# Kernel tuning notes

Measured on AMD Instinct MI355X. Metric: run time of the kernel, lower is better.

## Reference

```python
import jax, jax.numpy as jnp
import numpy as np

N, E, G = 50000, 1600000, 8
IN, H, C = 64, 4, 32
HID = H * C  # 128
L = 3


def setup_inputs() -> dict:
    key = jax.random.key(0)
    ks = jax.random.split(key, 20)
    x = jax.random.normal(ks[0], (N, IN), dtype=jnp.float32)
    edge_index = jax.random.randint(ks[1], (2, E), 0, N, dtype=jnp.int64)
    batch = jnp.sort(jax.random.randint(ks[2], (N,), 0, G, dtype=jnp.int64))
    s = 0.05
    Wp = jax.random.normal(ks[3], (IN, HID), dtype=jnp.float32) * s
    bp = jnp.zeros((HID,), dtype=jnp.float32)
    Wl = jax.random.normal(ks[4], (L, HID, HID), dtype=jnp.float32) * s
    att_src = jax.random.normal(ks[5], (L, H, C), dtype=jnp.float32) * s
    att_dst = jax.random.normal(ks[6], (L, H, C), dtype=jnp.float32) * s
    bconv = jnp.zeros((L, HID), dtype=jnp.float32)
    W1 = jax.random.normal(ks[7], (2 * HID, 256), dtype=jnp.float32) * s
    b1 = jnp.zeros((256,), dtype=jnp.float32)
    W2 = jax.random.normal(ks[8], (256, 128), dtype=jnp.float32) * s
    b2 = jnp.zeros((128,), dtype=jnp.float32)
    W3 = jax.random.normal(ks[9], (128, 1), dtype=jnp.float32) * s
    b3 = jnp.zeros((1,), dtype=jnp.float32)
    return dict(x=x, edge_index=edge_index, batch=batch, Wp=Wp, bp=bp, Wl=Wl,
                att_src=att_src, att_dst=att_dst, bconv=bconv,
                W1=W1, b1=b1, W2=W2, b2=b2, W3=W3, b3=b3)


def _gat_layer(x, src, dst, W, a_src, a_dst, b):
    # PyG GATConv (concat=True, add_self_loops handled by caller via src/dst)
    h = (x @ W).reshape(N, H, C)                      # [N,H,C]
    asrc = jnp.sum(h * a_src, axis=-1)                # [N,H]
    adst = jnp.sum(h * a_dst, axis=-1)                # [N,H]
    e = jax.nn.leaky_relu(asrc[src] + adst[dst], 0.2)  # [E',H]
    m = jax.ops.segment_max(e, dst, num_segments=N)   # scatter-softmax over dst
    e = jnp.exp(e - m[dst])
    z = jax.ops.segment_sum(e, dst, num_segments=N)
    alpha = e / (z[dst] + 1e-16)                      # [E',H]
    out = jax.ops.segment_sum(h[src] * alpha[:, :, None], dst, num_segments=N)
    return out.reshape(N, HID) + b


def reference(x, edge_index, batch, Wp, bp, Wl, att_src, att_dst, bconv,
              W1, b1, W2, b2, W3, b3):
    # add self loops once (PyG default add_self_loops=True)
    loop = jnp.arange(N, dtype=edge_index.dtype)
    src = jnp.concatenate([edge_index[0], loop])
    dst = jnp.concatenate([edge_index[1], loop])

    h = jax.nn.relu(x @ Wp + bp)
    for l in range(L):
        h = jax.nn.relu(_gat_layer(h, src, dst, Wl[l], att_src[l], att_dst[l], bconv[l]))

    cnt = jax.ops.segment_sum(jnp.ones((N,), h.dtype), batch, num_segments=G)
    mean = jax.ops.segment_sum(h, batch, num_segments=G) / jnp.maximum(cnt, 1.0)[:, None]
    mx = jax.ops.segment_max(h, batch, num_segments=G)
    mx = jnp.where(cnt[:, None] > 0, mx, 0.0)
    p = jnp.concatenate([mean, mx], axis=-1)          # [G, 2*HID]

    p = jax.nn.relu(p @ W1 + b1)
    p = jax.nn.relu(p @ W2 + b2)
    return (p @ W3 + b3).squeeze(-1)                  # [G]
```

## Files before the change

### kernel.cpp

```cpp
#include <hip/hip_runtime.h>
#include <math.h>

#define NN 50000
#define GG 8
#define HEADS 4
#define CH 32
#define HID 128
#define NLAYER 3
#define POOL_S 64
#define DEG_CAP 96
#define NBG2 ((NN + 63) / 64)
#define NBS 1024

__device__ float g_h[(size_t)NN * HID];
__device__ float g_h2[(size_t)NN * HID];
__device__ unsigned short g_h2b[(size_t)NN * HID];
__device__ float g_as[(size_t)NN * HEADS];
__device__ float g_ad[(size_t)NN * HEADS];
__device__ int g_cursor[NN];
__device__ unsigned short g_csr16[(size_t)NN * DEG_CAP];
__device__ int g_starts[GG + 1];
__device__ double g_psum[(size_t)GG * POOL_S * HID];
__device__ float g_pmax[(size_t)GG * POOL_S * HID];

__device__ __forceinline__ float lrelu(float v) { return v > 0.f ? v : 0.2f * v; }

__device__ __forceinline__ float bf2f(unsigned short u) {
    union { unsigned int i; float f; } v;
    v.i = ((unsigned int)u) << 16;
    return v.f;
}
__device__ __forceinline__ unsigned short f2bf(float f) {
    union { float f; unsigned int i; } v;
    v.f = f;
    unsigned int r = v.i + 0x7FFFu + ((v.i >> 16) & 1u);
    return (unsigned short)(r >> 16);
}

__global__ void zero_kernel() {
    int i = blockIdx.x * blockDim.x + threadIdx.x;
    if (i < NN) g_cursor[i] = 0;
}

template <int K, bool ATT, bool RELU, bool SRC_PARAM>
__device__ __forceinline__ void gemm_body(
    const float* __restrict__ Xp, const float* __restrict__ W, const float* __restrict__ bias,
    const float* __restrict__ att_s, const float* __restrict__ att_d, int n, int blk) {
    constexpr int KT = 32;
    constexpr int XS = 68;
    __shared__ float Ws[KT * 128];
    __shared__ float Xs[KT * XS];
    const float* X = SRC_PARAM ? Xp : g_h;
    float* Y = ATT ? g_h2 : g_h;
    int tid = threadIdx.x;
    int base = blk * 64;
    int rows = n - base;
    if (rows > 64) rows = 64;
    int cg = tid & 15, rg = tid >> 4;
    int c0 = cg * 8, r0 = rg * 4;
    float acc[4][8];
#pragma unroll
    for (int i = 0; i < 4; i++)
#pragma unroll
        for (int j = 0; j < 8; j++) acc[i][j] = 0.f;

    for (int kb = 0; kb < K; kb += KT) {
        {
            const float4* Wg = (const float4*)(W + (size_t)kb * 128);
            float4* Ws4 = (float4*)Ws;
#pragma unroll
            for (int u = 0; u < 4; u++) Ws4[tid + u * 256] = Wg[tid + u * 256];
        }
#pragma unroll
        for (int u = 0; u < 2; u++) {
            int i = tid + u * 256;
            int r = i >> 3, k4 = i & 7;
            float4 v = {0.f, 0.f, 0.f, 0.f};
            if (r < rows) v = *(const float4*)(X + (size_t)(base + r) * K + kb + k4 * 4);
            Xs[(k4 * 4 + 0) * XS + r] = v.x;
            Xs[(k4 * 4 + 1) * XS + r] = v.y;
            Xs[(k4 * 4 + 2) * XS + r] = v.z;
            Xs[(k4 * 4 + 3) * XS + r] = v.w;
        }
        __syncthreads();
#pragma unroll 8
        for (int k = 0; k < KT; k++) {
            const float4 xa = *(const float4*)&Xs[k * XS + r0];
            const float4 wa = *(const float4*)&Ws[k * 128 + c0];
            const float4 wb = *(const float4*)&Ws[k * 128 + c0 + 4];
            const float xr[4] = {xa.x, xa.y, xa.z, xa.w};
            const float wr[8] = {wa.x, wa.y, wa.z, wa.w, wb.x, wb.y, wb.z, wb.w};
#pragma unroll
            for (int ii = 0; ii < 4; ii++)
#pragma unroll
                for (int jj = 0; jj < 8; jj++) acc[ii][jj] += xr[ii] * wr[jj];
        }
        __syncthreads();
    }

    float bv[8];
#pragma unroll
    for (int j = 0; j < 8; j++) bv[j] = bias ? bias[c0 + j] : 0.f;
#pragma unroll
    for (int ii = 0; ii < 4; ii++) {
        int r = r0 + ii;
        if (r < rows) {
            float o[8];
#pragma unroll
            for (int jj = 0; jj < 8; jj++) {
                o[jj] = acc[ii][jj] + bv[jj];
                if (RELU) o[jj] = fmaxf(o[jj], 0.f);
            }
            float4 oa = {o[0], o[1], o[2], o[3]};
            float4 ob = {o[4], o[5], o[6], o[7]};
            *(float4*)&Y[(size_t)(base + r) * 128 + c0] = oa;
            *(float4*)&Y[(size_t)(base + r) * 128 + c0 + 4] = ob;
            if constexpr (ATT) {
                uint4 pk;
                pk.x = (unsigned)f2bf(o[0]) | ((unsigned)f2bf(o[1]) << 16);
                pk.y = (unsigned)f2bf(o[2]) | ((unsigned)f2bf(o[3]) << 16);
                pk.z = (unsigned)f2bf(o[4]) | ((unsigned)f2bf(o[5]) << 16);
                pk.w = (unsigned)f2bf(o[6]) | ((unsigned)f2bf(o[7]) << 16);
                *(uint4*)&g_h2b[(size_t)(base + r) * 128 + c0] = pk;
            }
        }
    }

    if constexpr (ATT) {
        float avs[8], avd[8];
#pragma unroll
        for (int j = 0; j < 8; j++) { avs[j] = att_s[c0 + j]; avd[j] = att_d[c0 + j]; }
#pragma unroll
        for (int ii = 0; ii < 4; ii++) {
            float ps = 0.f, pd = 0.f;
#pragma unroll
            for (int jj = 0; jj < 8; jj++) { ps += acc[ii][jj] * avs[jj]; pd += acc[ii][jj] * avd[jj]; }
            ps += __shfl_xor(ps, 1); ps += __shfl_xor(ps, 2);
            pd += __shfl_xor(pd, 1); pd += __shfl_xor(pd, 2);
            int r = r0 + ii;
            if ((cg & 3) == 0 && r < rows) {
                g_as[(size_t)(base + r) * 4 + (cg >> 2)] = ps;
                g_ad[(size_t)(base + r) * 4 + (cg >> 2)] = pd;
            }
        }
    }
}

template <int K, bool ATT, bool RELU, bool SRC_PARAM>
__global__ __launch_bounds__(256) void gemm_kernel(
    const float* __restrict__ Xp, const float* __restrict__ W, const float* __restrict__ bias,
    const float* __restrict__ att_s, const float* __restrict__ att_d, int n) {
    gemm_body<K, ATT, RELU, SRC_PARAM>(Xp, W, bias, att_s, att_d, n, blockIdx.x);
}

template <int K, bool ATT, bool RELU, bool SRC_PARAM>
__global__ __launch_bounds__(256) void fat_kernel(
    const float* __restrict__ Xp, const float* __restrict__ W, const float* __restrict__ bias,
    const float* __restrict__ as_, const float* __restrict__ ad_,
    const int* __restrict__ srcv, const int* __restrict__ dstv, int ebeg, int eend) {
    if (blockIdx.x < NBG2) {
        gemm_body<K, ATT, RELU, SRC_PARAM>(Xp, W, bias, as_, ad_, NN, blockIdx.x);
    } else {
        int idx = ebeg + (blockIdx.x - NBG2) * 256 + threadIdx.x;
        int stride = (gridDim.x - NBG2) * 256;
        for (int j = idx; j < eend; j += stride) {
            int d = dstv[j];
            int pos = atomicAdd(&g_cursor[d], 1);
            if (pos < DEG_CAP) g_csr16[(size_t)d * DEG_CAP + pos] = (unsigned short)srcv[j];
        }
    }
}

__global__ __launch_bounds__(256) void gat_layer_kernel(const float* __restrict__ bconv) {
    int wave = threadIdx.x >> 6;
    int lane = threadIdx.x & 63;
    int i = blockIdx.x * 4 + wave;

    int deg = g_cursor[i];
    if (deg > DEG_CAP) deg = DEG_CAP;

    int stream = lane >> 5;
    int sl = lane & 31;
    int hl = sl >> 3;
    int c0 = sl * 4;

    float ad_h = g_ad[(size_t)i * 4 + hl];
    const unsigned short* csr = &g_csr16[(size_t)i * DEG_CAP];

    float4 acc = {0.f, 0.f, 0.f, 0.f};
    float zacc = 0.f;

    int j = stream;
    for (; j + 14 < deg; j += 16) {
        int s0 = csr[j];      int s1 = csr[j + 2];  int s2 = csr[j + 4];  int s3 = csr[j + 6];
        int s4 = csr[j + 8];  int s5 = csr[j + 10]; int s6 = csr[j + 12]; int s7 = csr[j + 14];
        float a0 = g_as[(size_t)s0 * 4 + hl];
        float a1 = g_as[(size_t)s1 * 4 + hl];
        float a2 = g_as[(size_t)s2 * 4 + hl];
        float a3 = g_as[(size_t)s3 * 4 + hl];
        float a4 = g_as[(size_t)s4 * 4 + hl];
        float a5 = g_as[(size_t)s5 * 4 + hl];
        float a6 = g_as[(size_t)s6 * 4 + hl];
        float a7 = g_as[(size_t)s7 * 4 + hl];
        ushort4 q0 = *(const ushort4*)&g_h2b[(size_t)s0 * 128 + c0];
        ushort4 q1 = *(const ushort4*)&g_h2b[(size_t)s1 * 128 + c0];
        ushort4 q2 = *(const ushort4*)&g_h2b[(size_t)s2 * 128 + c0];
        ushort4 q3 = *(const ushort4*)&g_h2b[(size_t)s3 * 128 + c0];
        ushort4 q4 = *(const ushort4*)&g_h2b[(size_t)s4 * 128 + c0];
        ushort4 q5 = *(const ushort4*)&g_h2b[(size_t)s5 * 128 + c0];
        ushort4 q6 = *(const ushort4*)&g_h2b[(size_t)s6 * 128 + c0];
        ushort4 q7 = *(const ushort4*)&g_h2b[(size_t)s7 * 128 + c0];
        float w0 = expf(lrelu(a0 + ad_h));
        float w1 = expf(lrelu(a1 + ad_h));
        float w2 = expf(lrelu(a2 + ad_h));
        float w3 = expf(lrelu(a3 + ad_h));
        float w4 = expf(lrelu(a4 + ad_h));
        float w5 = expf(lrelu(a5 + ad_h));
        float w6 = expf(lrelu(a6 + ad_h));
        float w7 = expf(lrelu(a7 + ad_h));
        acc.x += w0 * bf2f(q0.x); acc.y += w0 * bf2f(q0.y); acc.z += w0 * bf2f(q0.z); acc.w += w0 * bf2f(q0.w);
        acc.x += w1 * bf2f(q1.x); acc.y += w1 * bf2f(q1.y); acc.z += w1 * bf2f(q1.z); acc.w += w1 * bf2f(q1.w);
        acc.x += w2 * bf2f(q2.x); acc.y += w2 * bf2f(q2.y); acc.z += w2 * bf2f(q2.z); acc.w += w2 * bf2f(q2.w);
        acc.x += w3 * bf2f(q3.x); acc.y += w3 * bf2f(q3.y); acc.z += w3 * bf2f(q3.z); acc.w += w3 * bf2f(q3.w);
        acc.x += w4 * bf2f(q4.x); acc.y += w4 * bf2f(q4.y); acc.z += w4 * bf2f(q4.z); acc.w += w4 * bf2f(q4.w);
        acc.x += w5 * bf2f(q5.x); acc.y += w5 * bf2f(q5.y); acc.z += w5 * bf2f(q5.z); acc.w += w5 * bf2f(q5.w);
        acc.x += w6 * bf2f(q6.x); acc.y += w6 * bf2f(q6.y); acc.z += w6 * bf2f(q6.z); acc.w += w6 * bf2f(q6.w);
        acc.x += w7 * bf2f(q7.x); acc.y += w7 * bf2f(q7.y); acc.z += w7 * bf2f(q7.z); acc.w += w7 * bf2f(q7.w);
        zacc += (w0 + w1) + (w2 + w3) + ((w4 + w5) + (w6 + w7));
    }
    for (; j < deg; j += 2) {
        int s = csr[j];
        float a = g_as[(size_t)s * 4 + hl];
        ushort4 q = *(const ushort4*)&g_h2b[(size_t)s * 128 + c0];
        float w = expf(lrelu(a + ad_h));
        acc.x += w * bf2f(q.x); acc.y += w * bf2f(q.y); acc.z += w * bf2f(q.z); acc.w += w * bf2f(q.w);
        zacc += w;
    }

    acc.x += __shfl_xor(acc.x, 32);
    acc.y += __shfl_xor(acc.y, 32);
    acc.z += __shfl_xor(acc.z, 32);
    acc.w += __shfl_xor(acc.w, 32);
    zacc  += __shfl_xor(zacc, 32);

    if (lane < 32) {
        float as_i = g_as[(size_t)i * 4 + hl];
        float sw = expf(lrelu(as_i + ad_h));
        float invz = 1.f / (zacc + sw + 1e-16f);
        float4 hv = *(const float4*)&g_h2[(size_t)i * 128 + c0];
        float4 bc = *(const float4*)&bconv[c0];
        float4 o;
        o.x = fmaxf((sw * hv.x + acc.x) * invz + bc.x, 0.f);
        o.y = fmaxf((sw * hv.y + acc.y) * invz + bc.y, 0.f);
        o.z = fmaxf((sw * hv.z + acc.z) * invz + bc.z, 0.f);
        o.w = fmaxf((sw * hv.w + acc.w) * invz + bc.w, 0.f);
        *(float4*)&g_h[(size_t)i * 128 + c0] = o;
    }
}

__global__ void bounds_kernel(const int* __restrict__ batch) {
    int t = threadIdx.x;
    if (t > GG) return;
    int lo = 0, hi = NN;
    while (lo < hi) {
        int mid = (lo + hi) >> 1;
        if (batch[mid] < t) lo = mid + 1; else hi = mid;
    }
    g_starts[t] = lo;
}

__global__ void pool1_kernel() {
    int g = blockIdx.x / POOL_S, s = blockIdx.x % POOL_S;
    int n0 = g_starts[g], n1 = g_starts[g + 1];
    long long cnt = n1 - n0;
    int a = n0 + (int)(cnt * s / POOL_S);
    int b = n0 + (int)(cnt * (s + 1) / POOL_S);
    int c = threadIdx.x;
    double sum = 0.0;
    float mx = -INFINITY;
    for (int nn = a; nn < b; nn++) {
        float v = g_h[(size_t)nn * 128 + c];
        sum += v;
        mx = fmaxf(mx, v);
    }
    g_psum[(size_t)blockIdx.x * 128 + c] = sum;
    g_pmax[(size_t)blockIdx.x * 128 + c] = mx;
}

__global__ __launch_bounds__(256) void head_kernel(
    const float* __restrict__ W1, const float* __restrict__ b1,
    const float* __restrict__ W2, const float* __restrict__ b2,
    const float* __restrict__ W3, const float* __restrict__ b3,
    float* __restrict__ outv) {
    __shared__ float p[256];
    __shared__ float r1[256];
    __shared__ float r2[128];
    int g = blockIdx.x, t = threadIdx.x;
    int cnt = g_starts[g + 1] - g_starts[g];
    if (t < 128) {
        double s = 0.0;
        for (int q = 0; q < POOL_S; q++) s += g_psum[(size_t)(g * POOL_S + q) * 128 + t];
        double dcnt = cnt > 0 ? (double)cnt : 1.0;
        p[t] = (float)(s / dcnt);
    } else {
        int c = t - 128;
        float mx = -INFINITY;
        for (int q = 0; q < POOL_S; q++) mx = fmaxf(mx, g_pmax[(size_t)(g * POOL_S + q) * 128 + c]);
        p[t] = cnt > 0 ? mx : 0.f;
    }
    __syncthreads();
    float acc = b1[t];
    for (int k = 0; k < 256; k++) acc += p[k] * W1[k * 256 + t];
    r1[t] = fmaxf(acc, 0.f);
    __syncthreads();
    if (t < 128) {
        float a2 = b2[t];
        for (int k = 0; k < 256; k++) a2 += r1[k] * W2[k * 128 + t];
        r2[t] = fmaxf(a2, 0.f);
    }
    __syncthreads();
    if (t < 64) {
        float a3 = r2[t] * W3[t] + r2[t + 64] * W3[t + 64];
#pragma unroll
        for (int d = 32; d >= 1; d >>= 1) a3 += __shfl_down(a3, d);
        if (t == 0) outv[g] = a3 + b3[0];
    }
}

extern "C" void kernel_launch(void* const* d_in, const int* in_sizes, int n_in,
                              void* d_out, int out_size, void* d_ws, size_t ws_size,
                              hipStream_t stream) {
    const float* x = (const float*)d_in[0];
    const int* eidx = (const int*)d_in[1];
    const int* batch = (const int*)d_in[2];
    const float* Wp = (const float*)d_in[3];
    const float* bp = (const float*)d_in[4];
    const float* Wl = (const float*)d_in[5];
    const float* att_src = (const float*)d_in[6];
    const float* att_dst = (const float*)d_in[7];
    const float* bconv = (const float*)d_in[8];
    const float* W1 = (const float*)d_in[9];
    const float* b1 = (const float*)d_in[10];
    const float* W2 = (const float*)d_in[11];
    const float* b2 = (const float*)d_in[12];
    const float* W3 = (const float*)d_in[13];
    const float* b3 = (const float*)d_in[14];
    float* out = (float*)d_out;
    int E = in_sizes[1] / 2;
    int Emid = E / 2;

    zero_kernel<<<(NN + 255) / 256, 256, 0, stream>>>();

    fat_kernel<64, false, true, true><<<NBG2 + NBS, 256, 0, stream>>>(
        x, Wp, bp, nullptr, nullptr, eidx, eidx + E, 0, Emid);

    fat_kernel<128, true, false, false><<<NBG2 + NBS, 256, 0, stream>>>(
        nullptr, Wl, nullptr, att_src, att_dst, eidx, eidx + E, Emid, E);

    gat_layer_kernel<<<NN / 4, 256, 0, stream>>>(bconv);

    for (int l = 1; l < NLAYER; l++) {
        gemm_kernel<128, true, false, false><<<NBG2, 256, 0, stream>>>(
            nullptr, Wl + (size_t)l * HID * HID, nullptr,
            att_src + (size_t)l * HEADS * CH, att_dst + (size_t)l * HEADS * CH, NN);
        gat_layer_kernel<<<NN / 4, 256, 0, stream>>>(bconv + (size_t)l * HID);
    }

    bounds_kernel<<<1, 64, 0, stream>>>(batch);
    pool1_kernel<<<GG * POOL_S, 128, 0, stream>>>();
    head_kernel<<<GG, 256, 0, stream>>>(W1, b1, W2, b2, W3, b3, out);
}
```

Measured before the change: 563.7 us.

## Drop fp32 projection buffer and share attention exps across lanes in GAT aggregation

The attention-projection GEMM no longer writes an fp32 copy of h; only the bf16 copy is stored, and the self-loop term reads it. In the aggregation loop, each stream loads its eight neighbor indices with one 16-byte load. Each lane computes one exp for a single neighbor/head and broadcasts it with shuffles, where before every lane recomputed all eight. This removes redundant exp work, scalar index loads and a 25 MB fp32 write per layer, at the cost of extra shuffles, a more complex tail path and bf16 rounding of the self-loop feature.

```diff
diff --git a/kernel.cpp b/kernel.cpp
--- a/kernel.cpp
+++ b/kernel.cpp
@@ -13,12 +13,11 @@
 #define NBS 1024
 
 __device__ float g_h[(size_t)NN * HID];
-__device__ float g_h2[(size_t)NN * HID];
-__device__ unsigned short g_h2b[(size_t)NN * HID];
+__device__ __attribute__((aligned(16))) unsigned short g_h2b[(size_t)NN * HID];
 __device__ float g_as[(size_t)NN * HEADS];
 __device__ float g_ad[(size_t)NN * HEADS];
 __device__ int g_cursor[NN];
-__device__ unsigned short g_csr16[(size_t)NN * DEG_CAP];
+__device__ __attribute__((aligned(16))) unsigned short g_csr16[(size_t)NN * DEG_CAP];
 __device__ int g_starts[GG + 1];
 __device__ double g_psum[(size_t)GG * POOL_S * HID];
 __device__ float g_pmax[(size_t)GG * POOL_S * HID];
@@ -51,7 +50,6 @@
     __shared__ float Ws[KT * 128];
     __shared__ float Xs[KT * XS];
     const float* X = SRC_PARAM ? Xp : g_h;
-    float* Y = ATT ? g_h2 : g_h;
     int tid = threadIdx.x;
     int base = blk * 64;
     int rows = n - base;
@@ -98,35 +96,39 @@
         __syncthreads();
     }
 
-    float bv[8];
-#pragma unroll
-    for (int j = 0; j < 8; j++) bv[j] = bias ? bias[c0 + j] : 0.f;
-#pragma unroll
-    for (int ii = 0; ii < 4; ii++) {
-        int r = r0 + ii;
-        if (r < rows) {
-            float o[8];
-#pragma unroll
-            for (int jj = 0; jj < 8; jj++) {
-                o[jj] = acc[ii][jj] + bv[jj];
-                if (RELU) o[jj] = fmaxf(o[jj], 0.f);
+    if constexpr (!ATT) {
+        float bv[8];
+#pragma unroll
+        for (int j = 0; j < 8; j++) bv[j] = bias ? bias[c0 + j] : 0.f;
+#pragma unroll
+        for (int ii = 0; ii < 4; ii++) {
+            int r = r0 + ii;
+            if (r < rows) {
+                float o[8];
+#pragma unroll
+                for (int jj = 0; jj < 8; jj++) {
+                    o[jj] = acc[ii][jj] + bv[jj];
+                    if (RELU) o[jj] = fmaxf(o[jj], 0.f);
+                }
+                float4 oa = {o[0], o[1], o[2], o[3]};
+                float4 ob = {o[4], o[5], o[6], o[7]};
+                *(float4*)&g_h[(size_t)(base + r) * 128 + c0] = oa;
+                *(float4*)&g_h[(size_t)(base + r) * 128 + c0 + 4] = ob;
             }
-            float4 oa = {o[0], o[1], o[2], o[3]};
-            float4 ob = {o[4], o[5], o[6], o[7]};
-            *(float4*)&Y[(size_t)(base + r) * 128 + c0] = oa;
-            *(float4*)&Y[(size_t)(base + r) * 128 + c0 + 4] = ob;
-            if constexpr (ATT) {
+        }
+    } else {
+#pragma unroll
+        for (int ii = 0; ii < 4; ii++) {
+            int r = r0 + ii;
+            if (r < rows) {
                 uint4 pk;
-                pk.x = (unsigned)f2bf(o[0]) | ((unsigned)f2bf(o[1]) << 16);
-                pk.y = (unsigned)f2bf(o[2]) | ((unsigned)f2bf(o[3]) << 16);
-                pk.z = (unsigned)f2bf(o[4]) | ((unsigned)f2bf(o[5]) << 16);
-                pk.w = (unsigned)f2bf(o[6]) | ((unsigned)f2bf(o[7]) << 16);
+                pk.x = (unsigned)f2bf(acc[ii][0]) | ((unsigned)f2bf(acc[ii][1]) << 16);
+                pk.y = (unsigned)f2bf(acc[ii][2]) | ((unsigned)f2bf(acc[ii][3]) << 16);
+                pk.z = (unsigned)f2bf(acc[ii][4]) | ((unsigned)f2bf(acc[ii][5]) << 16);
+                pk.w = (unsigned)f2bf(acc[ii][6]) | ((unsigned)f2bf(acc[ii][7]) << 16);
                 *(uint4*)&g_h2b[(size_t)(base + r) * 128 + c0] = pk;
             }
         }
-    }
-
-    if constexpr (ATT) {
         float avs[8], avd[8];
 #pragma unroll
         for (int j = 0; j < 8; j++) { avs[j] = att_s[c0 + j]; avd[j] = att_d[c0 + j]; }
@@ -182,42 +184,45 @@
     int stream = lane >> 5;
     int sl = lane & 31;
     int hl = sl >> 3;
+    int li = sl & 7;
     int c0 = sl * 4;
+    int bsel = lane & 56;
 
     float ad_h = g_ad[(size_t)i * 4 + hl];
     const unsigned short* csr = &g_csr16[(size_t)i * DEG_CAP];
 
     float4 acc = {0.f, 0.f, 0.f, 0.f};
-    float zacc = 0.f;
-
-    int j = stream;
-    for (; j + 14 < deg; j += 16) {
-        int s0 = csr[j];      int s1 = csr[j + 2];  int s2 = csr[j + 4];  int s3 = csr[j + 6];
-        int s4 = csr[j + 8];  int s5 = csr[j + 10]; int s6 = csr[j + 12]; int s7 = csr[j + 14];
-        float a0 = g_as[(size_t)s0 * 4 + hl];
-        float a1 = g_as[(size_t)s1 * 4 + hl];
-        float a2 = g_as[(size_t)s2 * 4 + hl];
-        float a3 = g_as[(size_t)s3 * 4 + hl];
-        float a4 = g_as[(size_t)s4 * 4 + hl];
-        float a5 = g_as[(size_t)s5 * 4 + hl];
-        float a6 = g_as[(size_t)s6 * 4 + hl];
-        float a7 = g_as[(size_t)s7 * 4 + hl];
-        ushort4 q0 = *(const ushort4*)&g_h2b[(size_t)s0 * 128 + c0];
-        ushort4 q1 = *(const ushort4*)&g_h2b[(size_t)s1 * 128 + c0];
-        ushort4 q2 = *(const ushort4*)&g_h2b[(size_t)s2 * 128 + c0];
-        ushort4 q3 = *(const ushort4*)&g_h2b[(size_t)s3 * 128 + c0];
-        ushort4 q4 = *(const ushort4*)&g_h2b[(size_t)s4 * 128 + c0];
-        ushort4 q5 = *(const ushort4*)&g_h2b[(size_t)s5 * 128 + c0];
-        ushort4 q6 = *(const ushort4*)&g_h2b[(size_t)s6 * 128 + c0];
-        ushort4 q7 = *(const ushort4*)&g_h2b[(size_t)s7 * 128 + c0];
-        float w0 = expf(lrelu(a0 + ad_h));
-        float w1 = expf(lrelu(a1 + ad_h));
-        float w2 = expf(lrelu(a2 + ad_h));
-        float w3 = expf(lrelu(a3 + ad_h));
-        float w4 = expf(lrelu(a4 + ad_h));
-        float w5 = expf(lrelu(a5 + ad_h));
-        float w6 = expf(lrelu(a6 + ad_h));
-        float w7 = expf(lrelu(a7 + ad_h));
+    float zraw = 0.f;
+
+    int nfull = deg >> 4;
+    for (int t = 0; t < nfull; ++t) {
+        int j0 = t * 16 + stream * 8;
+        uint4 cs = *(const uint4*)(csr + j0);
+        int s0 = cs.x & 0xFFFF, s1 = cs.x >> 16;
+        int s2 = cs.y & 0xFFFF, s3 = cs.y >> 16;
+        int s4 = cs.z & 0xFFFF, s5 = cs.z >> 16;
+        int s6 = cs.w & 0xFFFF, s7 = cs.w >> 16;
+        ushort4 q0 = *(const ushort4*)&g_h2b[(s0 << 7) + c0];
+        ushort4 q1 = *(const ushort4*)&g_h2b[(s1 << 7) + c0];
+        ushort4 q2 = *(const ushort4*)&g_h2b[(s2 << 7) + c0];
+        ushort4 q3 = *(const ushort4*)&g_h2b[(s3 << 7) + c0];
+        ushort4 q4 = *(const ushort4*)&g_h2b[(s4 << 7) + c0];
+        ushort4 q5 = *(const ushort4*)&g_h2b[(s5 << 7) + c0];
+        ushort4 q6 = *(const ushort4*)&g_h2b[(s6 << 7) + c0];
+        ushort4 q7 = *(const ushort4*)&g_h2b[(s7 << 7) + c0];
+        unsigned wsel = li < 4 ? (li < 2 ? cs.x : cs.y) : (li < 6 ? cs.z : cs.w);
+        int sm = (li & 1) ? (int)(wsel >> 16) : (int)(wsel & 0xFFFF);
+        float a = g_as[(sm << 2) + hl];
+        float wr = expf(lrelu(a + ad_h));
+        zraw += wr;
+        float w0 = __shfl(wr, bsel | 0);
+        float w1 = __shfl(wr, bsel | 1);
+        float w2 = __shfl(wr, bsel | 2);
+        float w3 = __shfl(wr, bsel | 3);
+        float w4 = __shfl(wr, bsel | 4);
+        float w5 = __shfl(wr, bsel | 5);
+        float w6 = __shfl(wr, bsel | 6);
+        float w7 = __shfl(wr, bsel | 7);
         acc.x += w0 * bf2f(q0.x); acc.y += w0 * bf2f(q0.y); acc.z += w0 * bf2f(q0.z); acc.w += w0 * bf2f(q0.w);
         acc.x += w1 * bf2f(q1.x); acc.y += w1 * bf2f(q1.y); acc.z += w1 * bf2f(q1.z); acc.w += w1 * bf2f(q1.w);
         acc.x += w2 * bf2f(q2.x); acc.y += w2 * bf2f(q2.y); acc.z += w2 * bf2f(q2.z); acc.w += w2 * bf2f(q2.w);
@@ -226,34 +231,42 @@
         acc.x += w5 * bf2f(q5.x); acc.y += w5 * bf2f(q5.y); acc.z += w5 * bf2f(q5.z); acc.w += w5 * bf2f(q5.w);
         acc.x += w6 * bf2f(q6.x); acc.y += w6 * bf2f(q6.y); acc.z += w6 * bf2f(q6.z); acc.w += w6 * bf2f(q6.w);
         acc.x += w7 * bf2f(q7.x); acc.y += w7 * bf2f(q7.y); acc.z += w7 * bf2f(q7.z); acc.w += w7 * bf2f(q7.w);
-        zacc += (w0 + w1) + (w2 + w3) + ((w4 + w5) + (w6 + w7));
-    }
-    for (; j < deg; j += 2) {
-        int s = csr[j];
-        float a = g_as[(size_t)s * 4 + hl];
-        ushort4 q = *(const ushort4*)&g_h2b[(size_t)s * 128 + c0];
-        float w = expf(lrelu(a + ad_h));
-        acc.x += w * bf2f(q.x); acc.y += w * bf2f(q.y); acc.z += w * bf2f(q.z); acc.w += w * bf2f(q.w);
-        zacc += w;
+    }
+
+    int tbase = nfull * 16 + stream * 8;
+#pragma unroll
+    for (int k = 0; k < 8; ++k) {
+        if (tbase + k < deg) {
+            int s = csr[tbase + k];
+            float a = g_as[(s << 2) + hl];
+            float wr = expf(lrelu(a + ad_h));
+            zraw += wr * 0.125f;
+            ushort4 q = *(const ushort4*)&g_h2b[(s << 7) + c0];
+            acc.x += wr * bf2f(q.x); acc.y += wr * bf2f(q.y);
+            acc.z += wr * bf2f(q.z); acc.w += wr * bf2f(q.w);
+        }
     }
 
     acc.x += __shfl_xor(acc.x, 32);
     acc.y += __shfl_xor(acc.y, 32);
     acc.z += __shfl_xor(acc.z, 32);
     acc.w += __shfl_xor(acc.w, 32);
-    zacc  += __shfl_xor(zacc, 32);
+    zraw += __shfl_xor(zraw, 1);
+    zraw += __shfl_xor(zraw, 2);
+    zraw += __shfl_xor(zraw, 4);
+    zraw += __shfl_xor(zraw, 32);
 
     if (lane < 32) {
-        float as_i = g_as[(size_t)i * 4 + hl];
+        float as_i = g_as[(i << 2) + hl];
         float sw = expf(lrelu(as_i + ad_h));
-        float invz = 1.f / (zacc + sw + 1e-16f);
-        float4 hv = *(const float4*)&g_h2[(size_t)i * 128 + c0];
+        float invz = 1.f / (zraw + sw + 1e-16f);
+        ushort4 qs = *(const ushort4*)&g_h2b[(i << 7) + c0];
         float4 bc = *(const float4*)&bconv[c0];
         float4 o;
-        o.x = fmaxf((sw * hv.x + acc.x) * invz + bc.x, 0.f);
-        o.y = fmaxf((sw * hv.y + acc.y) * invz + bc.y, 0.f);
-        o.z = fmaxf((sw * hv.z + acc.z) * invz + bc.z, 0.f);
-        o.w = fmaxf((sw * hv.w + acc.w) * invz + bc.w, 0.f);
+        o.x = fmaxf((sw * bf2f(qs.x) + acc.x) * invz + bc.x, 0.f);
+        o.y = fmaxf((sw * bf2f(qs.y) + acc.y) * invz + bc.y, 0.f);
+        o.z = fmaxf((sw * bf2f(qs.z) + acc.z) * invz + bc.z, 0.f);
+        o.w = fmaxf((sw * bf2f(qs.w) + acc.w) * invz + bc.w, 0.f);
         *(float4*)&g_h[(size_t)i * 128 + c0] = o;
     }
 }
```

Measured after the change: 533.4 us, median of 2. 5.4% less time.
